# Optimization experiments

Measured on AMD Instinct MI355X. Metric: run time of the kernel, lower is better.

## Reference

```python
import jax, jax.numpy as jnp
import numpy as np

B, S, D = 1024, 256, 128  # batch, seq_len, emb_dim; concat feat = 4*D = 512
H1, H2 = 256, 64          # att_hidden_size tail; att_hidden_size = [4*D, H1, H2]


def setup_inputs() -> dict:
    key = jax.random.key(0)
    ks = jax.random.split(key, 8)
    queries = jax.random.normal(ks[0], (B, D), dtype=jnp.float32)
    keys = jax.random.normal(ks[1], (B, S, D), dtype=jnp.float32)
    keys_length = jax.random.randint(ks[2], (B,), 1, S + 1)  # in [1, S]
    W1 = jax.random.normal(ks[3], (4 * D, H1), dtype=jnp.float32) * (1.0 / np.sqrt(4 * D))
    b1 = jnp.zeros((H1,), dtype=jnp.float32)
    W2 = jax.random.normal(ks[4], (H1, H2), dtype=jnp.float32) * (1.0 / np.sqrt(H1))
    b2 = jnp.zeros((H2,), dtype=jnp.float32)
    Wd = jax.random.normal(ks[5], (H2, 1), dtype=jnp.float32) * (1.0 / np.sqrt(H2))
    bd = jnp.zeros((1,), dtype=jnp.float32)
    return {"queries": queries, "keys": keys, "keys_length": keys_length,
            "W1": W1, "b1": b1, "W2": W2, "b2": b2, "Wd": Wd, "bd": bd}


def reference(queries, keys, keys_length, W1, b1, W2, b2, Wd, bd):
    # broadcast query across sequence: [B, S, D]
    q = jnp.broadcast_to(queries[:, None, :], keys.shape)
    feat = jnp.concatenate([q, keys, q - keys, q * keys], axis=-1)
    # att MLP (sigmoid after each layer, as in MLPLayers)
    h = jax.nn.sigmoid(jnp.einsum('bsf,fh->bsh', feat, W1) + b1)
    h = jax.nn.sigmoid(jnp.einsum('bsh,hk->bsk', h, W2) + b2)
    score = (jnp.einsum('bsk,ko->bso', h, Wd) + bd)[..., 0]  # [B, S]
    # mask: positions >= keys_length are invalid (mask_mat = arange(S))
    mask = jnp.arange(S)[None, :] >= keys_length[:, None]
    score = jnp.where(mask, -jnp.inf, score)  # softmax_stag=True -> -inf fill
    score = score / jnp.sqrt(jnp.float32(D))
    w = jax.nn.softmax(score, axis=1)  # [B, S]
    # return_seq_weight=False -> weighted sum over keys: [B, 1, D]
    out = jnp.einsum('bs,bsd->bd', w, keys)[:, None, :]
    return out
```

## Files before the change

### kernel.cpp

```cpp
#include <hip/hip_runtime.h>


typedef unsigned short u16;
typedef unsigned int u32;
typedef short bf16x8 __attribute__((ext_vector_type(8)));
typedef float f32x4 __attribute__((ext_vector_type(4)));

#define NBATCH 1024
#define SLEN 256
#define DD 128
#define NH1 256
#define NH2 64

#define WS_WBCT  0
#define WS_WDT   65536
#define WS_W2T   131072
#define WS_WDS   163840
#define WS_WSUM  165888
#define WS_BIAS1 296960

__device__ __forceinline__ u16 f2bf_rne(float f){
  union { float f; unsigned u; } v; v.f = f;
  unsigned r = v.u + 0x7fffu + ((v.u >> 16) & 1u);
  return (u16)(r >> 16);
}
__device__ __forceinline__ u32 pack_trunc(float a, float b){
  return (__float_as_uint(a) >> 16) | (__float_as_uint(b) & 0xffff0000u);
}
__device__ __forceinline__ float b2fl(short s){
  return __uint_as_float(((u32)(u16)s) << 16);
}
__device__ __forceinline__ bf16x8 pack8(float4 a, float4 b){
  union { u32 u[4]; bf16x8 v; } o;
  o.u[0] = pack_trunc(a.x, a.y);
  o.u[1] = pack_trunc(a.z, a.w);
  o.u[2] = pack_trunc(b.x, b.y);
  o.u[3] = pack_trunc(b.z, b.w);
  return o.v;
}
__device__ __forceinline__ int swz(int byte){
  return byte ^ (((byte >> 9) & 7) << 4);
}
__device__ __forceinline__ float fsigmoid(float x){
  return __builtin_amdgcn_rcpf(1.f + __expf(-x));
}
typedef const __attribute__((address_space(1))) unsigned gu32;
typedef __attribute__((address_space(3))) unsigned lu32;
__device__ __forceinline__ void gload16(const void* g, void* lds){
  __builtin_amdgcn_global_load_lds((gu32*)g, (lu32*)lds, 16, 0, 0);
}
__device__ __forceinline__ void barrier_lds(){
  asm volatile("s_waitcnt lgkmcnt(0)" ::: "memory");
  __builtin_amdgcn_s_barrier();
  asm volatile("" ::: "memory");
}

__global__ void prep_weights(const float* __restrict__ W1, const float* __restrict__ W2,
                             const float* __restrict__ Wd, const float* __restrict__ bd,
                             u16* __restrict__ WbcT, u16* __restrict__ WdT,
                             u16* __restrict__ W2T, float* __restrict__ WdS,
                             float* __restrict__ Wsum){
  int n = blockIdx.x;
  int k = threadIdx.x;
  if (k < DD){
    WbcT[n * DD + k] = f2bf_rne(W1[(128 + k) * NH1 + n] - W1[(256 + k) * NH1 + n]);
    WdT [n * DD + k] = f2bf_rne(W1[(384 + k) * NH1 + n]);
    Wsum[k * NH1 + n] = W1[k * NH1 + n] + W1[(256 + k) * NH1 + n];
  }
  if (n < NH2) W2T[n * 256 + k] = f2bf_rne(W2[k * NH2 + n]);
  if (n == 0 && k < NH2) WdS[k] = Wd[k];
  if (n == 0 && k == NH2) WdS[NH2] = bd[0];
}

__global__ void prep_bias(const float* __restrict__ q, const float* __restrict__ Wsum,
                          const float* __restrict__ b1, float* __restrict__ bias1){
  __shared__ float qsh[DD];
  int b = blockIdx.x, j = threadIdx.x;
  if (j < DD) qsh[j] = q[b * DD + j];
  __syncthreads();
  float acc = b1[j];
  #pragma unroll 8
  for (int d = 0; d < DD; ++d)
    acc += qsh[d] * Wsum[d * NH1 + j];
  bias1[b * NH1 + j] = acc;
}

__global__ __launch_bounds__(256, 2)
void seqatt_main(const float* __restrict__ queries, const float* __restrict__ keys,
                 const int* __restrict__ keys_length,
                 const u16* __restrict__ WbcT, const u16* __restrict__ WdT,
                 const u16* __restrict__ W2Tg,
                 const float* __restrict__ WdS, const float* __restrict__ bias1g,
                 const float* __restrict__ b2g, float* __restrict__ out)
{
  __shared__ alignas(16) char smem[68160];
  float* scores = (float*)(smem + 65536);
  float* bias1s = (float*)(smem + 66560);
  float* b2s    = (float*)(smem + 67584);
  float* wds    = (float*)(smem + 67840);
  float* red4   = (float*)(smem + 68104);

  const int b = blockIdx.x;
  const int tid = threadIdx.x;
  const int lane = tid & 63;
  const int wave = tid >> 6;
  const int l15 = lane & 15;
  const int g   = lane >> 4;

  bias1s[tid] = bias1g[b * NH1 + tid];
  if (tid < 64) b2s[tid] = b2g[tid];
  if (tid < 65) wds[tid] = WdS[tid];
  const int klen = keys_length[b];
  const float* kbb = keys + (long)b * SLEN * DD;

  bf16x8 bfrag[4][4];
  {
    const float* qb = queries + b * DD;
    #pragma unroll
    for (int nt = 0; nt < 4; ++nt){
      int n = (wave << 6) + (nt << 4) + l15;
      #pragma unroll
      for (int kk = 0; kk < 4; ++kk){
        int k0 = (g << 3) + (kk << 5);
        bf16x8 bc = *(const bf16x8*)(WbcT + n * DD + k0);
        bf16x8 wd = *(const bf16x8*)(WdT  + n * DD + k0);
        float4 q0 = *(const float4*)(qb + k0);
        float4 q1 = *(const float4*)(qb + k0 + 4);
        float qa[8] = {q0.x, q0.y, q0.z, q0.w, q1.x, q1.y, q1.z, q1.w};
        union { u16 s[8]; bf16x8 v; } o;
        #pragma unroll
        for (int j = 0; j < 8; ++j)
          o.s[j] = f2bf_rne(fmaf(qa[j], b2fl(wd[j]), b2fl(bc[j])));
        bfrag[nt][kk] = o.v;
      }
    }
  }
  bf16x8 w2frag[4][2];
  #pragma unroll
  for (int nt = 0; nt < 4; ++nt)
    #pragma unroll
    for (int kk2 = 0; kk2 < 2; ++kk2)
      w2frag[nt][kk2] = *(const bf16x8*)(W2Tg + ((nt << 4) + l15) * 256 + (wave << 6) + (kk2 << 5) + (g << 3));

  #pragma unroll
  for (int c = 0; c < 4; ++c){
    int n = c * 256 + (wave << 6) + lane;
    int u = swz(n * 16);
    gload16(kbb + (u >> 9) * DD + ((u >> 4) & 31) * 4,
            smem + ((c * 256 + (wave << 6)) * 16));
  }
  barrier_lds();

  const f32x4 fz = {0.f, 0.f, 0.f, 0.f};

  for (int st = 0; st < 8; ++st){
    const int s0 = st * 32;
    const int kb_base = (st & 1) * 16384;

    if (st < 7){
      const int nb = ((st + 1) & 1) * 16384;
      #pragma unroll
      for (int c = 0; c < 4; ++c){
        int n = c * 256 + (wave << 6) + lane;
        int u = swz(n * 16);
        gload16(kbb + (s0 + 32 + (u >> 9)) * DD + ((u >> 4) & 31) * 4,
                smem + (nb + (c * 256 + (wave << 6)) * 16));
      }
      asm volatile("s_waitcnt vmcnt(4) lgkmcnt(0)" ::: "memory");
    } else {
      asm volatile("s_waitcnt vmcnt(0) lgkmcnt(0)" ::: "memory");
    }
    __builtin_amdgcn_s_barrier();
    __builtin_amdgcn_sched_barrier(0);

    f32x4 acc[2][4];
    #pragma unroll
    for (int mt = 0; mt < 2; ++mt)
      #pragma unroll
      for (int nt = 0; nt < 4; ++nt) acc[mt][nt] = fz;
    #pragma unroll
    for (int kk = 0; kk < 4; ++kk){
      bf16x8 af[2];
      #pragma unroll
      for (int mt = 0; mt < 2; ++mt){
        int fb = kb_base + ((mt << 4) + l15) * 512 + (kk << 7) + (g << 5);
        float4 a = *(const float4*)(smem + swz(fb));
        float4 c4 = *(const float4*)(smem + swz(fb + 16));
        af[mt] = pack8(a, c4);
      }
      #pragma unroll
      for (int mt = 0; mt < 2; ++mt)
        #pragma unroll
        for (int nt = 0; nt < 4; ++nt)
          acc[mt][nt] = __builtin_amdgcn_mfma_f32_16x16x32_bf16(af[mt], bfrag[nt][kk], acc[mt][nt], 0, 0, 0);
    }

    #pragma unroll
    for (int nt = 0; nt < 4; ++nt){
      int h = (wave << 6) + (nt << 4) + l15;
      float bia = bias1s[h];
      #pragma unroll
      for (int mt = 0; mt < 2; ++mt)
        #pragma unroll
        for (int i = 0; i < 4; ++i){
          int row = (mt << 4) + (g << 2) + i;
          float hv = fsigmoid(acc[mt][nt][i] + bia);
          *(u16*)(smem + swz(32768 + row * 512 + h * 2)) = f2bf_rne(hv);
        }
    }
    asm volatile("s_waitcnt lgkmcnt(0)" ::: "memory");
    __builtin_amdgcn_s_barrier();
    __builtin_amdgcn_sched_barrier(0);

    f32x4 acc2[2][4];
    #pragma unroll
    for (int mt = 0; mt < 2; ++mt)
      #pragma unroll
      for (int nt = 0; nt < 4; ++nt) acc2[mt][nt] = fz;
    #pragma unroll
    for (int kk2 = 0; kk2 < 2; ++kk2){
      int kb = ((wave << 6) + (kk2 << 5) + (g << 3)) * 2;
      bf16x8 a2[2];
      #pragma unroll
      for (int mt = 0; mt < 2; ++mt)
        a2[mt] = *(const bf16x8*)(smem + swz(32768 + ((mt << 4) + l15) * 512 + kb));
      #pragma unroll
      for (int mt = 0; mt < 2; ++mt)
        #pragma unroll
        for (int nt = 0; nt < 4; ++nt)
          acc2[mt][nt] = __builtin_amdgcn_mfma_f32_16x16x32_bf16(a2[mt], w2frag[nt][kk2], acc2[mt][nt], 0, 0, 0);
    }
    {
      char* rbase = smem + 49152 + (wave << 12);
      #pragma unroll
      for (int mt = 0; mt < 2; ++mt)
        #pragma unroll
        for (int nt = 0; nt < 4; ++nt)
          #pragma unroll
          for (int i = 0; i < 4; ++i){
            int row = (mt << 4) + (g << 2) + i;
            *(u16*)(rbase + (row << 7) + (((nt << 4) + l15) << 1)) =
                (u16)(__float_as_uint(acc2[mt][nt][i]) >> 16);
          }
    }
    asm volatile("s_waitcnt lgkmcnt(0)" ::: "memory");
    __builtin_amdgcn_s_barrier();
    __builtin_amdgcn_sched_barrier(0);

    {
      int r = tid >> 3, og = tid & 7;
      const char* rb = smem + 49152 + (r << 7) + (og << 4);
      bf16x8 v0 = *(const bf16x8*)(rb);
      bf16x8 v1 = *(const bf16x8*)(rb + 4096);
      bf16x8 v2 = *(const bf16x8*)(rb + 8192);
      bf16x8 v3 = *(const bf16x8*)(rb + 12288);
      float p = 0.f;
      #pragma unroll
      for (int j = 0; j < 8; ++j){
        int o = (og << 3) + j;
        float s4 = (b2fl(v0[j]) + b2fl(v1[j])) + (b2fl(v2[j]) + b2fl(v3[j]));
        p += fsigmoid(s4 + b2s[o]) * wds[o];
      }
      p += __shfl_xor(p, 1);
      p += __shfl_xor(p, 2);
      p += __shfl_xor(p, 4);
      if (og == 0){
        int s = s0 + r;
        float sc = (p + wds[64]) * 0.08838834764831845f;
        scores[s] = (s < klen) ? sc : -1e30f;
      }
    }
  }

  barrier_lds();

  {
    float v = scores[tid];
    float m = v;
    #pragma unroll
    for (int off = 32; off >= 1; off >>= 1) m = fmaxf(m, __shfl_xor(m, off));
    if (lane == 0) red4[wave] = m;
    __syncthreads();
    float mx = fmaxf(fmaxf(red4[0], red4[1]), fmaxf(red4[2], red4[3]));
    float e = __expf(v - mx);
    float ssum = e;
    #pragma unroll
    for (int off = 32; off >= 1; off >>= 1) ssum += __shfl_xor(ssum, off);
    if (lane == 0) red4[4 + wave] = ssum;
    __syncthreads();
    float tot = red4[4] + red4[5] + red4[6] + red4[7];
    scores[tid] = e * __builtin_amdgcn_rcpf(tot);
    __syncthreads();
  }

  {
    float* red = (float*)(smem + 32768);
    int d = tid & 127, half = tid >> 7;
    const float* kb = keys + ((long)b * SLEN + half * 128) * DD + d;
    float acc = 0.f;
    #pragma unroll 4
    for (int s2 = 0; s2 < 128; ++s2) acc += scores[half * 128 + s2] * kb[s2 * DD];
    red[tid] = acc;
    __syncthreads();
    if (tid < 128) out[b * DD + tid] = red[tid] + red[128 + tid];
  }
}

extern "C" void kernel_launch(void* const* d_in, const int* in_sizes, int n_in,
                              void* d_out, int out_size, void* d_ws, size_t ws_size,
                              hipStream_t stream) {
  const float* queries     = (const float*)d_in[0];
  const float* keys        = (const float*)d_in[1];
  const int*   keys_length = (const int*)d_in[2];
  const float* W1 = (const float*)d_in[3];
  const float* b1 = (const float*)d_in[4];
  const float* W2 = (const float*)d_in[5];
  const float* b2 = (const float*)d_in[6];
  const float* Wd = (const float*)d_in[7];
  const float* bd = (const float*)d_in[8];
  float* out = (float*)d_out;
  char* ws = (char*)d_ws;

  u16*   WbcT  = (u16*)(ws + WS_WBCT);
  u16*   WdT   = (u16*)(ws + WS_WDT);
  u16*   W2T   = (u16*)(ws + WS_W2T);
  float* WdS   = (float*)(ws + WS_WDS);
  float* Wsum  = (float*)(ws + WS_WSUM);
  float* bias1 = (float*)(ws + WS_BIAS1);

  prep_weights<<<dim3(256), dim3(256), 0, stream>>>(W1, W2, Wd, bd, WbcT, WdT, W2T, WdS, Wsum);
  prep_bias<<<dim3(NBATCH), dim3(256), 0, stream>>>(queries, Wsum, b1, bias1);
  seqatt_main<<<dim3(NBATCH), dim3(256), 0, stream>>>(queries, keys, keys_length,
                                                      WbcT, WdT, W2T, WdS, bias1, b2, out);
}
```

Baseline: 105.7 us.

## Shrink LDS footprint, transpose MFMA operands for packed stores, raise occupancy

Shrinks the main kernel's shared memory from about 68KB to about 52KB by reusing the hidden-layer buffer for the layer-2 partial results, and raises launch bounds to 3 blocks per CU. It swaps the MFMA A/B operands so each lane holds 4 consecutive hidden units of one row, which allows packed 8-byte stores with truncation in place of scattered 2-byte RNE stores. The layer-2 bias and output weights are now read with vector loads. Reusing the buffer requires an extra barrier before the partial-result write, and the tighter launch bound may force register spills.

```diff
diff --git a/kernel.cpp b/kernel.cpp
--- a/kernel.cpp
+++ b/kernel.cpp
@@ -18,6 +18,15 @@
 #define WS_WDS   163840
 #define WS_WSUM  165888
 #define WS_BIAS1 296960
+
+#define L_KBUF   0
+#define L_H1     32768
+#define L_SCORES 49152
+#define L_BIAS   50176
+#define L_B2     51200
+#define L_WD     51456
+#define L_RED4   51728
+#define L_SIZE   51776
 
 __device__ __forceinline__ u16 f2bf_rne(float f){
   union { float f; unsigned u; } v; v.f = f;
@@ -52,7 +61,7 @@
 __device__ __forceinline__ void barrier_lds(){
   asm volatile("s_waitcnt lgkmcnt(0)" ::: "memory");
   __builtin_amdgcn_s_barrier();
-  asm volatile("" ::: "memory");
+  __builtin_amdgcn_sched_barrier(0);
 }
 
 __global__ void prep_weights(const float* __restrict__ W1, const float* __restrict__ W2,
@@ -85,7 +94,7 @@
   bias1[b * NH1 + j] = acc;
 }
 
-__global__ __launch_bounds__(256, 2)
+__global__ __launch_bounds__(256, 3)
 void seqatt_main(const float* __restrict__ queries, const float* __restrict__ keys,
                  const int* __restrict__ keys_length,
                  const u16* __restrict__ WbcT, const u16* __restrict__ WdT,
@@ -93,12 +102,12 @@
                  const float* __restrict__ WdS, const float* __restrict__ bias1g,
                  const float* __restrict__ b2g, float* __restrict__ out)
 {
-  __shared__ alignas(16) char smem[68160];
-  float* scores = (float*)(smem + 65536);
-  float* bias1s = (float*)(smem + 66560);
-  float* b2s    = (float*)(smem + 67584);
-  float* wds    = (float*)(smem + 67840);
-  float* red4   = (float*)(smem + 68104);
+  __shared__ alignas(16) char smem[L_SIZE];
+  float* scores = (float*)(smem + L_SCORES);
+  float* bias1s = (float*)(smem + L_BIAS);
+  float* b2s    = (float*)(smem + L_B2);
+  float* wds    = (float*)(smem + L_WD);
+  float* red4   = (float*)(smem + L_RED4);
 
   const int b = blockIdx.x;
   const int tid = threadIdx.x;
@@ -192,24 +201,25 @@
       for (int mt = 0; mt < 2; ++mt)
         #pragma unroll
         for (int nt = 0; nt < 4; ++nt)
-          acc[mt][nt] = __builtin_amdgcn_mfma_f32_16x16x32_bf16(af[mt], bfrag[nt][kk], acc[mt][nt], 0, 0, 0);
+          acc[mt][nt] = __builtin_amdgcn_mfma_f32_16x16x32_bf16(bfrag[nt][kk], af[mt], acc[mt][nt], 0, 0, 0);
     }
 
     #pragma unroll
     for (int nt = 0; nt < 4; ++nt){
-      int h = (wave << 6) + (nt << 4) + l15;
-      float bia = bias1s[h];
-      #pragma unroll
-      for (int mt = 0; mt < 2; ++mt)
-        #pragma unroll
-        for (int i = 0; i < 4; ++i){
-          int row = (mt << 4) + (g << 2) + i;
-          float hv = fsigmoid(acc[mt][nt][i] + bia);
-          *(u16*)(smem + swz(32768 + row * 512 + h * 2)) = f2bf_rne(hv);
-        }
+      float4 bia = *(const float4*)(bias1s + (wave << 6) + (nt << 4) + (g << 2));
+      #pragma unroll
+      for (int mt = 0; mt < 2; ++mt){
+        float v0 = fsigmoid(acc[mt][nt][0] + bia.x);
+        float v1 = fsigmoid(acc[mt][nt][1] + bia.y);
+        float v2 = fsigmoid(acc[mt][nt][2] + bia.z);
+        float v3 = fsigmoid(acc[mt][nt][3] + bia.w);
+        uint2 p; p.x = pack_trunc(v0, v1); p.y = pack_trunc(v2, v3);
+        int s = (mt << 4) + l15;
+        int hb = (wave << 6) + (nt << 4) + (g << 2);
+        *(uint2*)(smem + swz(L_H1 + s * 512 + hb * 2)) = p;
+      }
     }
     asm volatile("s_waitcnt lgkmcnt(0)" ::: "memory");
-    __builtin_amdgcn_s_barrier();
     __builtin_amdgcn_sched_barrier(0);
 
     f32x4 acc2[2][4];
@@ -223,43 +233,46 @@
       bf16x8 a2[2];
       #pragma unroll
       for (int mt = 0; mt < 2; ++mt)
-        a2[mt] = *(const bf16x8*)(smem + swz(32768 + ((mt << 4) + l15) * 512 + kb));
+        a2[mt] = *(const bf16x8*)(smem + swz(L_H1 + ((mt << 4) + l15) * 512 + kb));
       #pragma unroll
       for (int mt = 0; mt < 2; ++mt)
         #pragma unroll
         for (int nt = 0; nt < 4; ++nt)
-          acc2[mt][nt] = __builtin_amdgcn_mfma_f32_16x16x32_bf16(a2[mt], w2frag[nt][kk2], acc2[mt][nt], 0, 0, 0);
-    }
-    {
-      char* rbase = smem + 49152 + (wave << 12);
-      #pragma unroll
-      for (int mt = 0; mt < 2; ++mt)
-        #pragma unroll
-        for (int nt = 0; nt < 4; ++nt)
-          #pragma unroll
-          for (int i = 0; i < 4; ++i){
-            int row = (mt << 4) + (g << 2) + i;
-            *(u16*)(rbase + (row << 7) + (((nt << 4) + l15) << 1)) =
-                (u16)(__float_as_uint(acc2[mt][nt][i]) >> 16);
-          }
-    }
-    asm volatile("s_waitcnt lgkmcnt(0)" ::: "memory");
-    __builtin_amdgcn_s_barrier();
-    __builtin_amdgcn_sched_barrier(0);
+          acc2[mt][nt] = __builtin_amdgcn_mfma_f32_16x16x32_bf16(w2frag[nt][kk2], a2[mt], acc2[mt][nt], 0, 0, 0);
+    }
+    barrier_lds();
+
+    #pragma unroll
+    for (int mt = 0; mt < 2; ++mt)
+      #pragma unroll
+      for (int nt = 0; nt < 4; ++nt){
+        uint2 p;
+        p.x = pack_trunc(acc2[mt][nt][0], acc2[mt][nt][1]);
+        p.y = pack_trunc(acc2[mt][nt][2], acc2[mt][nt][3]);
+        int s = (mt << 4) + l15;
+        int ob = (nt << 4) + (g << 2);
+        *(uint2*)(smem + swz(L_H1 + (wave << 12) + (s << 7) + ob * 2)) = p;
+      }
+    barrier_lds();
 
     {
       int r = tid >> 3, og = tid & 7;
-      const char* rb = smem + 49152 + (r << 7) + (og << 4);
-      bf16x8 v0 = *(const bf16x8*)(rb);
-      bf16x8 v1 = *(const bf16x8*)(rb + 4096);
-      bf16x8 v2 = *(const bf16x8*)(rb + 8192);
-      bf16x8 v3 = *(const bf16x8*)(rb + 12288);
+      const int rb0 = L_H1 + (r << 7) + (og << 4);
+      bf16x8 v0 = *(const bf16x8*)(smem + swz(rb0));
+      bf16x8 v1 = *(const bf16x8*)(smem + swz(rb0 + 4096));
+      bf16x8 v2 = *(const bf16x8*)(smem + swz(rb0 + 8192));
+      bf16x8 v3 = *(const bf16x8*)(smem + swz(rb0 + 12288));
+      float4 b2a = *(const float4*)(b2s + (og << 3));
+      float4 b2b = *(const float4*)(b2s + (og << 3) + 4);
+      float4 wda = *(const float4*)(wds + (og << 3));
+      float4 wdb = *(const float4*)(wds + (og << 3) + 4);
+      float ba[8] = {b2a.x, b2a.y, b2a.z, b2a.w, b2b.x, b2b.y, b2b.z, b2b.w};
+      float wa[8] = {wda.x, wda.y, wda.z, wda.w, wdb.x, wdb.y, wdb.z, wdb.w};
       float p = 0.f;
       #pragma unroll
       for (int j = 0; j < 8; ++j){
-        int o = (og << 3) + j;
         float s4 = (b2fl(v0[j]) + b2fl(v1[j])) + (b2fl(v2[j]) + b2fl(v3[j]));
-        p += fsigmoid(s4 + b2s[o]) * wds[o];
+        p += fsigmoid(s4 + ba[j]) * wa[j];
       }
       p += __shfl_xor(p, 1);
       p += __shfl_xor(p, 2);
@@ -294,7 +307,7 @@
   }
 
   {
-    float* red = (float*)(smem + 32768);
+    float* red = (float*)smem;
     int d = tid & 127, half = tid >> 7;
     const float* kb = keys + ((long)b * SLEN + half * 128) * DD + d;
     float acc = 0.f;
```

After: 159.9 us. +51.3%, slower.
